# Performance work log

Measured on AMD Instinct MI355X. Metric: run time of the kernel, lower is better.

The kernel has to match this reference:

```python
import jax, jax.numpy as jnp
import numpy as np

BN_EPS = 1e-5

def hardswish(z):
    return z * jnp.clip(z + 3.0, 0.0, 6.0) * (1.0 / 6.0)

def setup_inputs() -> dict:
    key = jax.random.key(0)
    k1, k2, k3, k4, k5, k6 = jax.random.split(key, 6)
    B, C, T, V, K = 64, 128, 256, 25, 3
    x = jax.random.normal(k1, (B, C, T, V), dtype=jnp.float32)
    A_fixed = jax.random.uniform(k2, (K, V, V), dtype=jnp.float32)
    A_learned = jax.random.normal(k3, (K, V, V), dtype=jnp.float32) * 0.01
    W_gcn = jax.random.normal(k4, (K, C, C), dtype=jnp.float32) * (1.0 / np.sqrt(C))
    bn_gamma = jax.random.uniform(k5, (C,), dtype=jnp.float32, minval=0.5, maxval=1.5)
    bn_beta = jax.random.normal(k6, (C,), dtype=jnp.float32) * 0.1
    return {"x": x, "A_fixed": A_fixed, "A_learned": A_learned,
            "W_gcn": W_gcn, "bn_gamma": bn_gamma, "bn_beta": bn_beta}

def reference(x, A_fixed, A_learned, W_gcn, bn_gamma, bn_beta):
    # x: [B,C,T,V]; A_*: [K,V,V]; W_gcn: [K,Cout,Cin]
    K = A_fixed.shape[0]
    # EfficientGCN-exact learnable graph: A_k = D^{-1/2} |A_fixed + A_learned| D^{-1/2}
    A_comb = jnp.abs(A_fixed + A_learned)                      # [K,V,V]
    d = jnp.clip(A_comb.sum(axis=2), 1e-6) ** -0.5             # row-degree^{-1/2}, [K,V]
    A_norm = d[:, :, None] * A_comb * d[:, None, :]            # [K,V,V]
    # x_flat @ A_norm per k  (contract over source joint v)
    x_k = jnp.einsum('bctv,kvw->kbctw', x, A_norm)             # [K,B,C,T,V]
    # K parallel 1x1 convs, averaged over k
    y = jnp.einsum('kbctv,koc->botv', x_k, W_gcn) / K          # [B,Cout,T,V]
    # eval-mode BatchNorm2d (running_mean=0, running_var=1)
    scale = bn_gamma / jnp.sqrt(1.0 + BN_EPS)
    y = y * scale[None, :, None, None] + bn_beta[None, :, None, None]
    y = hardswish(y)
    # DepthwiseSepTCN / DropPath treated as identity (eval, source truncated);
    # residual is Identity since in_ch==out_ch, stride==1
    return hardswish(y + x)
```

## Files before the change

kernel.cpp:

```cpp
#include <hip/hip_runtime.h>
#include <math.h>

#define BN_EPS 1e-5f

typedef __attribute__((ext_vector_type(4))) float f32x4;
typedef __attribute__((ext_vector_type(8))) __bf16 bf16x8;
typedef __attribute__((ext_vector_type(4))) unsigned int u32x4;

static __device__ __forceinline__ float hswish(float z){
    float c = fminf(fmaxf(z + 3.0f, 0.0f), 6.0f);
    return z * c * (1.0f/6.0f);
}
static __device__ __forceinline__ unsigned short bf16bits(float f){
    unsigned int u = __builtin_bit_cast(unsigned int, f);
    unsigned int r = u + 0x7FFFu + ((u >> 16) & 1u);
    return (unsigned short)(r >> 16);
}
static __device__ __forceinline__ float bf16f(unsigned short h){
    return __builtin_bit_cast(float, ((unsigned int)h) << 16);
}

__global__ void prep_A(const float* __restrict__ Af, const float* __restrict__ Al,
                       float* __restrict__ Atv){
    int k = blockIdx.x;
    __shared__ float Ac[25][25];
    __shared__ float dpow[25];
    int tid = threadIdx.x;
    for (int i = tid; i < 625; i += blockDim.x){
        float a = Af[k*625 + i] + Al[k*625 + i];
        Ac[i/25][i%25] = fabsf(a);
    }
    __syncthreads();
    if (tid < 25){
        float s = 0.f;
        #pragma unroll
        for (int w = 0; w < 25; ++w) s += Ac[tid][w];
        s = fmaxf(s, 1e-6f);
        dpow[tid] = 1.0f / sqrtf(s);
    }
    __syncthreads();
    for (int i = tid; i < 625; i += blockDim.x){
        int v = i/25, w = i%25;
        Atv[(k*25 + v)*32 + w] = dpow[v] * Ac[v][w] * dpow[w];
    }
}

__global__ void prep_W(const float* __restrict__ W, const float* __restrict__ gamma,
                       unsigned int* __restrict__ Wf){
    int fidx = blockIdx.x;
    int ot = fidx & 7, c0 = (fidx >> 3) & 3, k = fidx >> 5;
    int l = threadIdx.x;
    int o = ot*16 + (l & 15);
    int cb = c0*32 + ((l >> 4) << 3);
    float scale = gamma[o] * rsqrtf(1.0f + BN_EPS) * (1.0f/3.0f);
    const float* wr = W + (k*128 + o)*128 + cb;
    unsigned int p0, p1, p2, p3;
    p0 = (unsigned int)bf16bits(wr[0]*scale) | ((unsigned int)bf16bits(wr[1]*scale) << 16);
    p1 = (unsigned int)bf16bits(wr[2]*scale) | ((unsigned int)bf16bits(wr[3]*scale) << 16);
    p2 = (unsigned int)bf16bits(wr[4]*scale) | ((unsigned int)bf16bits(wr[5]*scale) << 16);
    p3 = (unsigned int)bf16bits(wr[6]*scale) | ((unsigned int)bf16bits(wr[7]*scale) << 16);
    u32x4 v = {p0, p1, p2, p3};
    ((u32x4*)Wf)[fidx*64 + l] = v;
}

__global__ __launch_bounds__(512, 4) void gcn_main(
    const float* __restrict__ x, const float* __restrict__ Atv,
    const unsigned int* __restrict__ Wf, const float* __restrict__ beta,
    float* __restrict__ out){
    extern __shared__ char smem[];
    unsigned short* lds16 = (unsigned short*)smem;
    const int XS = 24576;
    const int tile = blockIdx.x;
    const int b    = blockIdx.y;
    const int tid  = threadIdx.x;
    const int lane = tid & 63;
    const int wv   = tid >> 6;
    const int m0g  = tile * 50;
    const int t0   = tile * 2;

    {
        int xbase = (b*128)*6400 + t0*25;
        for (int j = tid; j < 6400; j += 512){
            int c = j / 50, tv = j - c*50;
            float f = x[xbase + c*6400 + tv];
            lds16[XS + c*54 + tv] = bf16bits(f);
        }
    }
    __syncthreads();

    for (int task = wv; task < 12; task += 8){
        int kk   = __builtin_amdgcn_readfirstlane(task >> 2);
        int tloc = __builtin_amdgcn_readfirstlane((task >> 1) & 1);
        int ch   = task & 1;
        int c = ch*64 + lane;
        float pacc[25];
        #pragma unroll
        for (int w = 0; w < 25; ++w) pacc[w] = 0.f;
        const float* Ak = Atv + kk*800;
        #pragma unroll 5
        for (int v = 0; v < 25; ++v){
            float xv = bf16f(lds16[XS + c*54 + tloc*25 + v]);
            const float* Ar = Ak + v*32;
            #pragma unroll
            for (int w = 0; w < 25; ++w)
                pacc[w] = fmaf(xv, Ar[w], pacc[w]);
        }
        #pragma unroll
        for (int w = 0; w < 25; ++w){
            int m = tloc*25 + w;
            int hw = m*384 + kk*128 + c;
            int byteoff = (hw << 1) ^ ((m & 7) << 4);
            *(unsigned short*)(smem + byteoff) = bf16bits(pacc[w]);
        }
    }
    __syncthreads();

    const int mh = wv >> 2;
    const int oq = wv & 3;
    const int r = lane & 15, g = lane >> 4;
    const int swz = (r & 7) << 4;
    f32x4 acc00 = {0.f,0.f,0.f,0.f}, acc01 = {0.f,0.f,0.f,0.f};
    f32x4 acc10 = {0.f,0.f,0.f,0.f}, acc11 = {0.f,0.f,0.f,0.f};
    const int abU0 = (mh*32 + r) * 768 + g*16;
    const int abU1 = abU0 + 16*768;
    const u32x4* WfV = (const u32x4*)Wf;
    const int ot0 = oq*2, ot1 = ot0 + 1;
    u32x4 b0 = WfV[(ot0)*64 + lane];
    u32x4 b1 = WfV[(ot1)*64 + lane];
    #pragma unroll
    for (int ks = 0; ks < 12; ++ks){
        u32x4 nb0 = b0, nb1 = b1;
        if (ks < 11){
            nb0 = WfV[((ks+1)*8 + ot0)*64 + lane];
            nb1 = WfV[((ks+1)*8 + ot1)*64 + lane];
        }
        bf16x8 a0 = *(const bf16x8*)(smem + ((abU0 + ks*64) ^ swz));
        bf16x8 a1 = *(const bf16x8*)(smem + ((abU1 + ks*64) ^ swz));
        bf16x8 f0 = __builtin_bit_cast(bf16x8, b0);
        bf16x8 f1 = __builtin_bit_cast(bf16x8, b1);
        acc00 = __builtin_amdgcn_mfma_f32_16x16x32_bf16(a0, f0, acc00, 0, 0, 0);
        acc01 = __builtin_amdgcn_mfma_f32_16x16x32_bf16(a0, f1, acc01, 0, 0, 0);
        acc10 = __builtin_amdgcn_mfma_f32_16x16x32_bf16(a1, f0, acc10, 0, 0, 0);
        acc11 = __builtin_amdgcn_mfma_f32_16x16x32_bf16(a1, f1, acc11, 0, 0, 0);
        b0 = nb0; b1 = nb1;
    }
    __syncthreads();

    {
        float* outst = (float*)smem;
        #pragma unroll
        for (int e = 0; e < 4; ++e){
            int o0 = oq*32 + r, o1 = o0 + 16;
            int mA = mh*32 + g*4 + e, mB = mA + 16;
            outst[o0*65 + mA] = acc00[e];
            outst[o1*65 + mA] = acc01[e];
            outst[o0*65 + mB] = acc10[e];
            outst[o1*65 + mB] = acc11[e];
        }
    }
    __syncthreads();

    {
        const float* outst = (const float*)smem;
        int o = tid >> 2, q = tid & 3;
        float bet = beta[o];
        int obase = (b*128 + o)*6400 + m0g;
        int nj = (q < 3) ? 8 : 1;
        for (int j2 = 0; j2 < nj; ++j2){
            int m = q*16 + 2*j2;
            float v0 = outst[o*65 + m];
            float v1 = outst[o*65 + m + 1];
            float2 xr = *(const float2*)(x + obase + m);
            float r0 = hswish(hswish(v0 + bet) + xr.x);
            float r1 = hswish(hswish(v1 + bet) + xr.y);
            float2 res = {r0, r1};
            *(float2*)(out + obase + m) = res;
        }
    }
}

extern "C" void kernel_launch(void* const* d_in, const int* in_sizes, int n_in,
                              void* d_out, int out_size, void* d_ws, size_t ws_size,
                              hipStream_t stream) {
    const float* x      = (const float*)d_in[0];
    const float* Afix   = (const float*)d_in[1];
    const float* Alrn   = (const float*)d_in[2];
    const float* Wg     = (const float*)d_in[3];
    const float* gamma  = (const float*)d_in[4];
    const float* beta   = (const float*)d_in[5];
    float* out = (float*)d_out;

    float* Atv = (float*)d_ws;
    unsigned int* Wf = (unsigned int*)((char*)d_ws + 16384);

    (void)hipFuncSetAttribute((const void*)gcn_main,
                              hipFuncAttributeMaxDynamicSharedMemorySize, 62976);

    prep_A<<<dim3(3), 256, 0, stream>>>(Afix, Alrn, Atv);
    prep_W<<<dim3(96), 64, 0, stream>>>(Wg, gamma, Wf);
    gcn_main<<<dim3(128, 64), 512, 62976, stream>>>(x, Atv, Wf, beta, out);
}
```

Measured before the change: 680.1 us.

## Compute graph aggregation with split-bf16 MFMA instead of scalar FMAs

Replaces the per-lane scalar 25x25 joint-mixing loop with 32x32x16 bf16 MFMA instructions. The normalized adjacency is split into hi/lo bf16 parts in a new prep kernel to keep accuracy near fp32. x is loaded straight from global into MFMA A-fragments, which removes the x LDS staging area, so dynamic shared memory drops from 62976 to 49152 bytes and occupancy can rise. In exchange the x loads are now per-row strided global reads, and MFMA work is wasted on padding (25 of 32 joints used).

Result: faster. 584.4 us (-14.1%).

```diff
diff --git a/kernel.cpp b/kernel.cpp
--- a/kernel.cpp
+++ b/kernel.cpp
@@ -3,9 +3,11 @@
 
 #define BN_EPS 1e-5f
 
-typedef __attribute__((ext_vector_type(4))) float f32x4;
-typedef __attribute__((ext_vector_type(8))) __bf16 bf16x8;
-typedef __attribute__((ext_vector_type(4))) unsigned int u32x4;
+typedef __attribute__((ext_vector_type(4)))  float f32x4;
+typedef __attribute__((ext_vector_type(16))) float f32x16;
+typedef __attribute__((ext_vector_type(8)))  __bf16 bf16x8;
+typedef __attribute__((ext_vector_type(8)))  unsigned short u16x8;
+typedef __attribute__((ext_vector_type(4)))  unsigned int u32x4;
 
 static __device__ __forceinline__ float hswish(float z){
     float c = fminf(fmaxf(z + 3.0f, 0.0f), 6.0f);
@@ -43,6 +45,28 @@
         int v = i/25, w = i%25;
         Atv[(k*25 + v)*32 + w] = dpow[v] * Ac[v][w] * dpow[w];
     }
+}
+
+__global__ void prep_Afrag(const float* __restrict__ Atv, u32x4* __restrict__ Af2){
+    int blk  = blockIdx.x;
+    int k    = blk >> 1, half = blk & 1;
+    int l    = threadIdx.x;
+    int w    = l & 31, g = l >> 5;
+    unsigned short hi[8], lo[8];
+    #pragma unroll
+    for (int i = 0; i < 8; ++i){
+        int v = half*16 + g*8 + i;
+        float val = (v < 25 && w < 25) ? Atv[(k*25 + v)*32 + w] : 0.f;
+        unsigned short h = bf16bits(val);
+        hi[i] = h;
+        lo[i] = bf16bits(val - bf16f(h));
+    }
+    u32x4 H = { (unsigned)hi[0] | ((unsigned)hi[1]<<16), (unsigned)hi[2] | ((unsigned)hi[3]<<16),
+                (unsigned)hi[4] | ((unsigned)hi[5]<<16), (unsigned)hi[6] | ((unsigned)hi[7]<<16) };
+    u32x4 L = { (unsigned)lo[0] | ((unsigned)lo[1]<<16), (unsigned)lo[2] | ((unsigned)lo[3]<<16),
+                (unsigned)lo[4] | ((unsigned)lo[5]<<16), (unsigned)lo[6] | ((unsigned)lo[7]<<16) };
+    Af2[(blk*2 + 0)*64 + l] = H;
+    Af2[(blk*2 + 1)*64 + l] = L;
 }
 
 __global__ void prep_W(const float* __restrict__ W, const float* __restrict__ gamma,
@@ -64,12 +88,10 @@
 }
 
 __global__ __launch_bounds__(512, 4) void gcn_main(
-    const float* __restrict__ x, const float* __restrict__ Atv,
+    const float* __restrict__ x, const u32x4* __restrict__ Af2,
     const unsigned int* __restrict__ Wf, const float* __restrict__ beta,
     float* __restrict__ out){
     extern __shared__ char smem[];
-    unsigned short* lds16 = (unsigned short*)smem;
-    const int XS = 24576;
     const int tile = blockIdx.x;
     const int b    = blockIdx.y;
     const int tid  = threadIdx.x;
@@ -79,38 +101,56 @@
     const int t0   = tile * 2;
 
     {
-        int xbase = (b*128)*6400 + t0*25;
-        for (int j = tid; j < 6400; j += 512){
-            int c = j / 50, tv = j - c*50;
-            float f = x[xbase + c*6400 + tv];
-            lds16[XS + c*54 + tv] = bf16bits(f);
-        }
-    }
-    __syncthreads();
-
-    for (int task = wv; task < 12; task += 8){
-        int kk   = __builtin_amdgcn_readfirstlane(task >> 2);
-        int tloc = __builtin_amdgcn_readfirstlane((task >> 1) & 1);
-        int ch   = task & 1;
-        int c = ch*64 + lane;
-        float pacc[25];
-        #pragma unroll
-        for (int w = 0; w < 25; ++w) pacc[w] = 0.f;
-        const float* Ak = Atv + kk*800;
-        #pragma unroll 5
-        for (int v = 0; v < 25; ++v){
-            float xv = bf16f(lds16[XS + c*54 + tloc*25 + v]);
-            const float* Ar = Ak + v*32;
+        const int c32 = wv & 3, tt = wv >> 2;
+        const int lw  = lane & 31, g5 = lane >> 5;
+        const int c   = c32*32 + lw;
+        const float* xrow = x + (((size_t)(b*128 + c)*256 + (t0 + tt))*25);
+
+        float a0f[8], a1f[8];
+        #pragma unroll
+        for (int i = 0; i < 8; ++i) a0f[i] = xrow[g5*8 + i];
+        if (g5 == 0){
             #pragma unroll
-            for (int w = 0; w < 25; ++w)
-                pacc[w] = fmaf(xv, Ar[w], pacc[w]);
-        }
-        #pragma unroll
-        for (int w = 0; w < 25; ++w){
-            int m = tloc*25 + w;
-            int hw = m*384 + kk*128 + c;
-            int byteoff = (hw << 1) ^ ((m & 7) << 4);
-            *(unsigned short*)(smem + byteoff) = bf16bits(pacc[w]);
+            for (int i = 0; i < 8; ++i) a1f[i] = xrow[16 + i];
+        } else {
+            a1f[0] = xrow[24];
+            #pragma unroll
+            for (int i = 1; i < 8; ++i) a1f[i] = 0.f;
+        }
+        u16x8 ua0, ua1;
+        #pragma unroll
+        for (int i = 0; i < 8; ++i){ ua0[i] = bf16bits(a0f[i]); ua1[i] = bf16bits(a1f[i]); }
+        bf16x8 A0 = __builtin_bit_cast(bf16x8, ua0);
+        bf16x8 A1 = __builtin_bit_cast(bf16x8, ua1);
+
+        const int mrow  = tt*25 + lw;
+        const int mbyte = mrow * 768;
+        const int swzb  = (mrow & 7) << 4;
+
+        for (int k = 0; k < 3; ++k){
+            u32x4 B0h = Af2[((k*2+0)*2 + 0)*64 + lane];
+            u32x4 B0l = Af2[((k*2+0)*2 + 1)*64 + lane];
+            u32x4 B1h = Af2[((k*2+1)*2 + 0)*64 + lane];
+            u32x4 B1l = Af2[((k*2+1)*2 + 1)*64 + lane];
+            f32x16 acc;
+            #pragma unroll
+            for (int e = 0; e < 16; ++e) acc[e] = 0.f;
+            acc = __builtin_amdgcn_mfma_f32_32x32x16_bf16(A1, __builtin_bit_cast(bf16x8, B1l), acc, 0,0,0);
+            acc = __builtin_amdgcn_mfma_f32_32x32x16_bf16(A0, __builtin_bit_cast(bf16x8, B0l), acc, 0,0,0);
+            acc = __builtin_amdgcn_mfma_f32_32x32x16_bf16(A1, __builtin_bit_cast(bf16x8, B1h), acc, 0,0,0);
+            acc = __builtin_amdgcn_mfma_f32_32x32x16_bf16(A0, __builtin_bit_cast(bf16x8, B0h), acc, 0,0,0);
+            if (lw < 25){
+                #pragma unroll
+                for (int q = 0; q < 4; ++q){
+                    int rowD = 8*q + 4*g5;
+                    int kc   = k*128 + c32*32 + rowD;
+                    unsigned int d0 = (unsigned int)bf16bits(acc[4*q+0]) | ((unsigned int)bf16bits(acc[4*q+1]) << 16);
+                    unsigned int d1 = (unsigned int)bf16bits(acc[4*q+2]) | ((unsigned int)bf16bits(acc[4*q+3]) << 16);
+                    int byteoff = (mbyte + kc*2) ^ swzb;
+                    uint2 vv = {d0, d1};
+                    *(uint2*)(smem + byteoff) = vv;
+                }
+            }
         }
     }
     __syncthreads();
@@ -190,13 +230,15 @@
     const float* beta   = (const float*)d_in[5];
     float* out = (float*)d_out;
 
-    float* Atv = (float*)d_ws;
-    unsigned int* Wf = (unsigned int*)((char*)d_ws + 16384);
+    float*        Atv = (float*)d_ws;
+    unsigned int* Wf  = (unsigned int*)((char*)d_ws + 16384);
+    u32x4*        Af2 = (u32x4*)((char*)d_ws + 118784);
 
     (void)hipFuncSetAttribute((const void*)gcn_main,
-                              hipFuncAttributeMaxDynamicSharedMemorySize, 62976);
+                              hipFuncAttributeMaxDynamicSharedMemorySize, 49152);
 
     prep_A<<<dim3(3), 256, 0, stream>>>(Afix, Alrn, Atv);
+    prep_Afrag<<<dim3(6), 64, 0, stream>>>(Atv, Af2);
     prep_W<<<dim3(96), 64, 0, stream>>>(Wg, gamma, Wf);
-    gcn_main<<<dim3(128, 64), 512, 62976, stream>>>(x, Atv, Wf, beta, out);
-}
+    gcn_main<<<dim3(128, 64), 512, 49152, stream>>>(x, Af2, Wf, beta, out);
+}
```
